# Kernel tuning notes

Hardware: AMD Instinct MI355X
Metric: run time of the kernel (lower is better)

## Reference

```python
import jax, jax.numpy as jnp
import numpy as np

N = 100000   # nodes
E = 3200000  # edges (avg degree 32)
F = 128      # num_features
H = 256      # hidden_dim
D = 256      # embedding_dim
O = 2        # output_dim
BN_EPS = 1e-5


def _mk_layer(keys, fin, fmid, fout):
    kW1, kW2 = keys
    W1 = jax.random.normal(kW1, (fin, fmid), jnp.float32) / np.sqrt(fin)
    b1 = jnp.zeros((fmid,), jnp.float32)
    g = jnp.ones((fmid,), jnp.float32)
    be = jnp.zeros((fmid,), jnp.float32)
    mu = jnp.zeros((fmid,), jnp.float32)
    var = jnp.ones((fmid,), jnp.float32)
    W2 = jax.random.normal(kW2, (fmid, fout), jnp.float32) / np.sqrt(fmid)
    b2 = jnp.zeros((fout,), jnp.float32)
    return W1, b1, g, be, mu, var, W2, b2


def setup_inputs() -> dict:
    key = jax.random.key(0)
    ks = jax.random.split(key, 10)
    inp = {}
    inp["x"] = jax.random.normal(ks[0], (N, F), jnp.float32)
    inp["edge_index"] = jax.random.randint(ks[1], (2, E), 0, N, jnp.int32)
    names = ["W1", "b1", "g", "be", "mu", "var", "W2", "b2"]
    for pref, (fin, fmid, fout), kk in [
        ("l1", (F, H, H), (ks[2], ks[3])),
        ("l2", (H, H, H), (ks[4], ks[5])),
        ("l3", (H, H, D), (ks[6], ks[7])),
    ]:
        vals = _mk_layer(kk, fin, fmid, fout)
        for n, v in zip(names, vals):
            inp[f"{pref}_{n}"] = v
    inp["out_W"] = jax.random.normal(ks[8], (D, O), jnp.float32) / np.sqrt(D)
    inp["out_b"] = jnp.zeros((O,), jnp.float32)
    return inp


def gin_layer(h, src, dst, W1, b1, g, be, mu, var, W2, b2, final_relu):
    # GINConv (eps=0): z_i = x_i + sum_{j->i} x_j, then MLP(Linear-BN-ReLU-Linear[-ReLU])
    agg = jax.ops.segment_sum(h[src], dst, num_segments=N)
    z = h + agg
    z = z @ W1 + b1
    z = (z - mu) * jax.lax.rsqrt(var + BN_EPS) * g + be  # BatchNorm1d (inference)
    z = jax.nn.relu(z)
    z = z @ W2 + b2
    if final_relu:
        z = jax.nn.relu(z)
    return z


def reference(x, edge_index,
              l1_W1, l1_b1, l1_g, l1_be, l1_mu, l1_var, l1_W2, l1_b2,
              l2_W1, l2_b1, l2_g, l2_be, l2_mu, l2_var, l2_W2, l2_b2,
              l3_W1, l3_b1, l3_g, l3_be, l3_mu, l3_var, l3_W2, l3_b2,
              out_W, out_b):
    src, dst = edge_index[0], edge_index[1]
    h = gin_layer(x, src, dst, l1_W1, l1_b1, l1_g, l1_be, l1_mu, l1_var, l1_W2, l1_b2, True)
    h = gin_layer(h, src, dst, l2_W1, l2_b1, l2_g, l2_be, l2_mu, l2_var, l2_W2, l2_b2, True)
    h = gin_layer(h, src, dst, l3_W1, l3_b1, l3_g, l3_be, l3_mu, l3_var, l3_W2, l3_b2, False)
    return h @ out_W + out_b  # [N, O]
```

## Files before the change

kernel.cpp:

```cpp
#include <hip/hip_runtime.h>
#include <cstdint>
#include <cstddef>

#define N_NODES 100000
#define N_EDGES 3200000
#define MPAD    100096
#define HID     256
#define NBUCK   196
#define BSH     9
#define BSTRIDE 18432

typedef _Float16 f16;
typedef _Float16 f16x2 __attribute__((ext_vector_type(2)));
typedef _Float16 f16x8 __attribute__((ext_vector_type(8)));
typedef float    f32x4 __attribute__((ext_vector_type(4)));

union F16x2 { unsigned u; f16 h[2]; f16x2 v; };
__device__ inline void unpack2(unsigned u, float& a, float& b) {
    F16x2 x; x.u = u; a = (float)x.h[0]; b = (float)x.h[1];
}
__device__ inline unsigned pack2(float a, float b) {
    F16x2 x; x.h[0] = (f16)a; x.h[1] = (f16)b; return x.u;
}
__device__ inline f16x2 asv(unsigned u) { F16x2 x; x.u = u; return x.v; }

__global__ __launch_bounds__(256) void k_bucketA(const int* __restrict__ src,
                                                 const int* __restrict__ dst,
                                                 unsigned* __restrict__ pairs,
                                                 int* __restrict__ nb, int e) {
    __shared__ int hist[NBUCK];
    __shared__ int lbase[NBUCK];
    __shared__ int lcur[NBUCK];
    const int t = threadIdx.x;
    for (int i = t; i < NBUCK; i += 256) hist[i] = 0;
    __syncthreads();
    const int e0 = blockIdx.x * 4096;
    bool v[16]; int d[16], s[16];
#pragma unroll
    for (int i = 0; i < 16; ++i) {
        int idx = e0 + i * 256 + t;
        v[i] = idx < e;
        d[i] = v[i] ? dst[idx] : 0;
        s[i] = v[i] ? src[idx] : 0;
    }
#pragma unroll
    for (int i = 0; i < 16; ++i)
        if (v[i]) atomicAdd(&hist[d[i] >> BSH], 1);
    __syncthreads();
    for (int i = t; i < NBUCK; i += 256) {
        int h = hist[i];
        lbase[i] = h ? atomicAdd(&nb[i], h) : 0;
        lcur[i] = 0;
    }
    __syncthreads();
#pragma unroll
    for (int i = 0; i < 16; ++i) {
        if (v[i]) {
            int b = d[i] >> BSH;
            int p = atomicAdd(&lcur[b], 1);
            unsigned packed = ((unsigned)(d[i] & 511) << 17) | (unsigned)s[i];
            pairs[(size_t)b * BSTRIDE + lbase[b] + p] = packed;
        }
    }
}

__global__ void k_scan196(const int* __restrict__ nb, int* __restrict__ bbase,
                          int* __restrict__ rowptrN) {
    __shared__ int s[256];
    int t = threadIdx.x;
    int v = (t < NBUCK) ? nb[t] : 0;
    s[t] = v;
    __syncthreads();
    for (int off = 1; off < 256; off <<= 1) {
        int u = (t >= off) ? s[t - off] : 0;
        __syncthreads();
        s[t] += u;
        __syncthreads();
    }
    if (t < NBUCK) bbase[t] = s[t] - v;
    if (t == 0) *rowptrN = N_EDGES;
}

__global__ __launch_bounds__(256) void k_bucketB(const unsigned* __restrict__ pairs,
                                                 const int* __restrict__ nb,
                                                 const int* __restrict__ bbase,
                                                 int* __restrict__ rowptr,
                                                 int* __restrict__ colidx) {
    __shared__ int deg[512];
    __shared__ int sc[512];
    __shared__ int cur[512];
    const int b = blockIdx.x, t = threadIdx.x;
    const int cnt = nb[b], base = bbase[b];
    const unsigned* P = pairs + (size_t)b * BSTRIDE;
    deg[t] = 0; deg[t + 256] = 0;
    __syncthreads();
    for (int i = t; i < cnt; i += 256) atomicAdd(&deg[P[i] >> 17], 1);
    __syncthreads();
    sc[t] = deg[t]; sc[t + 256] = deg[t + 256];
    __syncthreads();
    for (int off = 1; off < 512; off <<= 1) {
        int a0 = (t >= off) ? sc[t - off] : 0;
        int a1 = (t + 256 >= off) ? sc[t + 256 - off] : 0;
        __syncthreads();
        sc[t] += a0; sc[t + 256] += a1;
        __syncthreads();
    }
    int node0 = b << BSH;
#pragma unroll
    for (int rep = 0; rep < 2; ++rep) {
        int i = t + rep * 256;
        int excl = base + sc[i] - deg[i];
        cur[i] = excl;
        int node = node0 + i;
        if (node < N_NODES) rowptr[node] = excl;
    }
    __syncthreads();
    for (int i = t; i < cnt; i += 256) {
        unsigned p = P[i];
        int pos = atomicAdd(&cur[p >> 17], 1);
        colidx[pos] = (int)(p & 0x1FFFF);
    }
}

__global__ void k_cvt(const float2* __restrict__ x, unsigned* __restrict__ o, int n) {
    int t = blockIdx.x * 256 + threadIdx.x;
    if (t < n) { float2 v = x[t]; o[t] = pack2(v.x, v.y); }
}

__global__ void k_foldw1(const float* __restrict__ W, const float* __restrict__ b1,
                         const float* __restrict__ gm, const float* __restrict__ bt,
                         const float* __restrict__ mu, const float* __restrict__ vr,
                         f16* __restrict__ Wt, float* __restrict__ bias, int K) {
    int t = blockIdx.x * 256 + threadIdx.x;
    if (t >= K * 256) return;
    int n = t & 255, k = t >> 8;
    float sc = gm[n] * rsqrtf(vr[n] + 1e-5f);
    Wt[n * K + k] = (f16)(W[t] * sc);
    if (k == 0) bias[n] = (b1[n] - mu[n]) * sc + bt[n];
}

__global__ void k_transb(const float* __restrict__ W, f16* __restrict__ Wt) {
    int t = blockIdx.x * 256 + threadIdx.x;
    int n = t & 255, k = t >> 8;
    Wt[n * 256 + k] = (f16)W[t];
}

__global__ void k_fold2(const float* __restrict__ W2, const float* __restrict__ b2,
                        const float* __restrict__ outW, const float* __restrict__ outb,
                        float* __restrict__ W2o, float* __restrict__ bo) {
    int k = threadIdx.x;
    float a0 = 0.f, a1 = 0.f;
    for (int j = 0; j < 256; ++j) {
        float w = W2[k * 256 + j];
        a0 += w * outW[j * 2 + 0];
        a1 += w * outW[j * 2 + 1];
    }
    W2o[k * 2 + 0] = a0;
    W2o[k * 2 + 1] = a1;
    if (k < 2) {
        float b = outb[k];
        for (int j = 0; j < 256; ++j) b += b2[j] * outW[j * 2 + k];
        bo[k] = b;
    }
}

__global__ void k_agg256(const uint2* __restrict__ h, const unsigned* __restrict__ h8,
                         const int* __restrict__ rp, const int* __restrict__ ci,
                         uint2* __restrict__ z, int n) {
    int gw = (blockIdx.x * 256 + threadIdx.x) >> 6;
    if (gw >= n) return;
    int lane = threadIdx.x & 63;
    const unsigned* h8l = h8 + lane;
    uint2 d = h[(size_t)gw * 64 + lane];
    float a0, a1, a2, a3;
    unpack2(d.x, a0, a1); unpack2(d.y, a2, a3);
    int s = rp[gw], e = rp[gw + 1];
    int p = s;
    for (; p + 7 < e; p += 8) {
        int j0 = ci[p],     j1 = ci[p + 1], j2 = ci[p + 2], j3 = ci[p + 3];
        int j4 = ci[p + 4], j5 = ci[p + 5], j6 = ci[p + 6], j7 = ci[p + 7];
        unsigned u0 = h8l[(size_t)j0 * 64], u1 = h8l[(size_t)j1 * 64];
        unsigned u2 = h8l[(size_t)j2 * 64], u3 = h8l[(size_t)j3 * 64];
        unsigned u4 = h8l[(size_t)j4 * 64], u5 = h8l[(size_t)j5 * 64];
        unsigned u6 = h8l[(size_t)j6 * 64], u7 = h8l[(size_t)j7 * 64];
#pragma unroll
        for (int q = 0; q < 8; ++q) {
            unsigned u = q == 0 ? u0 : q == 1 ? u1 : q == 2 ? u2 : q == 3 ? u3
                       : q == 4 ? u4 : q == 5 ? u5 : q == 6 ? u6 : u7;
            auto lo = __builtin_amdgcn_cvt_pk_f32_fp8(u, false);
            auto hi = __builtin_amdgcn_cvt_pk_f32_fp8(u, true);
            a0 += lo[0]; a1 += lo[1]; a2 += hi[0]; a3 += hi[1];
        }
    }
    for (; p < e; ++p) {
        unsigned u = h8l[(size_t)ci[p] * 64];
        auto lo = __builtin_amdgcn_cvt_pk_f32_fp8(u, false);
        auto hi = __builtin_amdgcn_cvt_pk_f32_fp8(u, true);
        a0 += lo[0]; a1 += lo[1]; a2 += hi[0]; a3 += hi[1];
    }
    uint2 o; o.x = pack2(a0, a1); o.y = pack2(a2, a3);
    z[(size_t)gw * 64 + lane] = o;
}

__global__ void k_agg128(const unsigned* __restrict__ h, const int* __restrict__ rp,
                         const int* __restrict__ ci, unsigned* __restrict__ z, int n) {
    int gw = (blockIdx.x * 256 + threadIdx.x) >> 6;
    if (gw >= n) return;
    int lane = threadIdx.x & 63;
    const unsigned* hl = h + lane;
    float a0, a1, t0, t1;
    unpack2(hl[(size_t)gw * 64], a0, a1);
    int s = rp[gw], e = rp[gw + 1];
    int p = s;
    for (; p + 7 < e; p += 8) {
        int j0 = ci[p],     j1 = ci[p + 1], j2 = ci[p + 2], j3 = ci[p + 3];
        int j4 = ci[p + 4], j5 = ci[p + 5], j6 = ci[p + 6], j7 = ci[p + 7];
        unsigned v0 = hl[(size_t)j0 * 64], v1 = hl[(size_t)j1 * 64];
        unsigned v2 = hl[(size_t)j2 * 64], v3 = hl[(size_t)j3 * 64];
        unsigned v4 = hl[(size_t)j4 * 64], v5 = hl[(size_t)j5 * 64];
        unsigned v6 = hl[(size_t)j6 * 64], v7 = hl[(size_t)j7 * 64];
        f16x2 sx = asv(v0);
        sx += asv(v1); sx += asv(v2); sx += asv(v3);
        sx += asv(v4); sx += asv(v5); sx += asv(v6); sx += asv(v7);
        a0 += (float)sx[0]; a1 += (float)sx[1];
    }
    for (; p < e; ++p) {
        unpack2(hl[(size_t)ci[p] * 64], t0, t1); a0 += t0; a1 += t1;
    }
    z[(size_t)gw * 64 + lane] = pack2(a0, a1);
}

template <int K, bool RELU, bool STORE8>
__global__ __launch_bounds__(256) void k_gemm(const f16* __restrict__ A,
                                              const f16* __restrict__ Bt,
                                              const float* __restrict__ bias,
                                              f16* __restrict__ C,
                                              unsigned char* __restrict__ C8) {
    __shared__ f16 As[128 * 64];
    __shared__ f16 Bs[128 * 64];
    const int tid = threadIdx.x;
    const int bm0 = blockIdx.x * 128;
    const int bn0 = blockIdx.y * 128;
    const int lane = tid & 63, wave = tid >> 6;
    const int quad = lane >> 4, l16 = lane & 15;
    const int wr = (wave >> 1) * 64, wc = (wave & 1) * 64;
    f32x4 acc[4][4] = {};
    const f16* Abase = A + (size_t)bm0 * K;
    const f16* Bbase = Bt + (size_t)bn0 * K;

    for (int k0 = 0; k0 < K; k0 += 64) {
#pragma unroll
        for (int i = 0; i < 4; ++i) {
            int c = i * 256 + tid;
            int m = c >> 3;
            int gg = (c & 7) ^ (m & 7);
            __builtin_amdgcn_global_load_lds(
                (const __attribute__((address_space(1))) unsigned int*)(Abase + (size_t)m * K + k0 + gg * 8),
                (__attribute__((address_space(3))) unsigned int*)(As + (size_t)c * 8), 16, 0, 0);
            __builtin_amdgcn_global_load_lds(
                (const __attribute__((address_space(1))) unsigned int*)(Bbase + (size_t)m * K + k0 + gg * 8),
                (__attribute__((address_space(3))) unsigned int*)(Bs + (size_t)c * 8), 16, 0, 0);
        }
        __syncthreads();
#pragma unroll
        for (int kk = 0; kk < 64; kk += 32) {
            const int gbase = kk >> 3;
            f16x8 af[4], bfv[4];
#pragma unroll
            for (int mi = 0; mi < 4; ++mi) {
                int m = wr + mi * 16 + l16;
                int slot = (gbase + quad) ^ (m & 7);
                af[mi] = *(const f16x8*)&As[(m * 8 + slot) * 8];
            }
#pragma unroll
            for (int ni = 0; ni < 4; ++ni) {
                int m = wc + ni * 16 + l16;
                int slot = (gbase + quad) ^ (m & 7);
                bfv[ni] = *(const f16x8*)&Bs[(m * 8 + slot) * 8];
            }
#pragma unroll
            for (int mi = 0; mi < 4; ++mi)
#pragma unroll
                for (int ni = 0; ni < 4; ++ni)
                    acc[mi][ni] = __builtin_amdgcn_mfma_f32_16x16x32_f16(af[mi], bfv[ni], acc[mi][ni], 0, 0, 0);
        }
        __syncthreads();
    }

    float bv[4];
#pragma unroll
    for (int ni = 0; ni < 4; ++ni) bv[ni] = bias[bn0 + wc + ni * 16 + l16];
#pragma unroll
    for (int mi = 0; mi < 4; ++mi) {
#pragma unroll
        for (int r = 0; r < 4; ++r) {
            size_t row = (size_t)(bm0 + wr + mi * 16 + quad * 4 + r);
            f16* crow = C + row * HID + bn0 + wc + l16;
            unsigned char* crow8 = STORE8 ? (C8 + row * HID + bn0 + wc + l16) : nullptr;
#pragma unroll
            for (int ni = 0; ni < 4; ++ni) {
                float v = acc[mi][ni][r] + bv[ni];
                if (RELU) v = fmaxf(v, 0.f);
                crow[ni * 16] = (f16)v;
                if (STORE8) {
                    int pk = __builtin_amdgcn_cvt_pk_fp8_f32(v, v, 0, false);
                    crow8[ni * 16] = (unsigned char)(pk & 0xff);
                }
            }
        }
    }
}

__global__ void k_head(const uint2* __restrict__ y, const float* __restrict__ W2o,
                       const float* __restrict__ bo, float* __restrict__ out, int n) {
    __shared__ float w[512];
    __shared__ float bb[2];
    int t = threadIdx.x;
    w[t] = W2o[t];
    w[t + 256] = W2o[t + 256];
    if (t < 2) bb[t] = bo[t];
    __syncthreads();
    int gw = (blockIdx.x * 256 + t) >> 6;
    if (gw >= n) return;
    int lane = t & 63;
    uint2 d = y[(size_t)gw * 64 + lane];
    float x0, x1, x2, x3;
    unpack2(d.x, x0, x1); unpack2(d.y, x2, x3);
    int k = lane * 4;
    float o0 = x0 * w[k * 2 + 0] + x1 * w[k * 2 + 2] + x2 * w[k * 2 + 4] + x3 * w[k * 2 + 6];
    float o1 = x0 * w[k * 2 + 1] + x1 * w[k * 2 + 3] + x2 * w[k * 2 + 5] + x3 * w[k * 2 + 7];
#pragma unroll
    for (int off = 32; off > 0; off >>= 1) {
        o0 += __shfl_down(o0, off);
        o1 += __shfl_down(o1, off);
    }
    if (lane == 0) {
        out[(size_t)gw * 2 + 0] = o0 + bb[0];
        out[(size_t)gw * 2 + 1] = o1 + bb[1];
    }
}

extern "C" void kernel_launch(void* const* d_in, const int* in_sizes, int n_in,
                              void* d_out, int out_size, void* d_ws, size_t ws_size,
                              hipStream_t stream) {
    const float* x    = (const float*)d_in[0];
    const int*   ei   = (const int*)d_in[1];
    const int*   esrc = ei;
    const int*   edst = ei + N_EDGES;
    const float* lw[3][8];
    for (int l = 0; l < 3; ++l)
        for (int j = 0; j < 8; ++j) lw[l][j] = (const float*)d_in[2 + l * 8 + j];
    const float* outW = (const float*)d_in[26];
    const float* outB = (const float*)d_in[27];

    char* base = (char*)d_ws;
    size_t off = 0;
    auto alloc = [&](size_t bytes) -> void* {
        void* r = base + off;
        off += (bytes + 255) & ~(size_t)255;
        return r;
    };
    f16* z  = (f16*)alloc((size_t)MPAD * 256 * 2);
    f16* y  = (f16*)alloc((size_t)MPAD * 256 * 2);
    f16* h  = (f16*)alloc((size_t)MPAD * 256 * 2);
    unsigned char* h8 = (unsigned char*)alloc((size_t)MPAD * 256);
    f16* xh = (f16*)alloc((size_t)MPAD * 128 * 2);
    f16* W1t[3]; float* bias1[3]; f16* W2t[2];
    W1t[0] = (f16*)alloc(256 * 128 * 2);
    W1t[1] = (f16*)alloc(256 * 256 * 2);
    W1t[2] = (f16*)alloc(256 * 256 * 2);
    for (int l = 0; l < 2; ++l) W2t[l] = (f16*)alloc(256 * 256 * 2);
    for (int l = 0; l < 3; ++l) bias1[l] = (float*)alloc(256 * 4);
    float* W2o = (float*)alloc(512 * 4);
    float* bo  = (float*)alloc(2 * 4);
    unsigned* pairs = (unsigned*)alloc((size_t)NBUCK * BSTRIDE * 4);
    int* nb     = (int*)alloc(NBUCK * 4);
    int* bbase  = (int*)alloc(NBUCK * 4);
    int* rowptr = (int*)alloc((size_t)(N_NODES + 1) * 4);
    int* colidx = (int*)alloc((size_t)N_EDGES * 4);

    hipMemsetAsync(nb, 0, NBUCK * 4, stream);
    k_bucketA<<<(N_EDGES + 4095) / 4096, 256, 0, stream>>>(esrc, edst, pairs, nb, N_EDGES);
    k_scan196<<<1, 256, 0, stream>>>(nb, bbase, rowptr + N_NODES);
    k_bucketB<<<NBUCK, 256, 0, stream>>>(pairs, nb, bbase, rowptr, colidx);

    k_cvt<<<(N_NODES * 64 + 255) / 256, 256, 0, stream>>>((const float2*)x, (unsigned*)xh, N_NODES * 64);
    k_foldw1<<<128, 256, 0, stream>>>(lw[0][0], lw[0][1], lw[0][2], lw[0][3], lw[0][4], lw[0][5], W1t[0], bias1[0], 128);
    k_foldw1<<<256, 256, 0, stream>>>(lw[1][0], lw[1][1], lw[1][2], lw[1][3], lw[1][4], lw[1][5], W1t[1], bias1[1], 256);
    k_foldw1<<<256, 256, 0, stream>>>(lw[2][0], lw[2][1], lw[2][2], lw[2][3], lw[2][4], lw[2][5], W1t[2], bias1[2], 256);
    k_transb<<<256, 256, 0, stream>>>(lw[0][6], W2t[0]);
    k_transb<<<256, 256, 0, stream>>>(lw[1][6], W2t[1]);
    k_fold2<<<1, 256, 0, stream>>>(lw[2][6], lw[2][7], outW, outB, W2o, bo);

    const dim3 ggrid(MPAD / 128, 2);
    const int WBLOCKS = (N_NODES + 3) / 4;

    k_agg128<<<WBLOCKS, 256, 0, stream>>>((const unsigned*)xh, rowptr, colidx, (unsigned*)z, N_NODES);
    k_gemm<128, true, false><<<ggrid, 256, 0, stream>>>(z, W1t[0], bias1[0], y, nullptr);
    k_gemm<256, true, true ><<<ggrid, 256, 0, stream>>>(y, W2t[0], lw[0][7], h, h8);
    k_agg256<<<WBLOCKS, 256, 0, stream>>>((const uint2*)h, (const unsigned*)h8, rowptr, colidx, (uint2*)z, N_NODES);
    k_gemm<256, true, false><<<ggrid, 256, 0, stream>>>(z, W1t[1], bias1[1], y, nullptr);
    k_gemm<256, true, true ><<<ggrid, 256, 0, stream>>>(y, W2t[1], lw[1][7], h, h8);
    k_agg256<<<WBLOCKS, 256, 0, stream>>>((const uint2*)h, (const unsigned*)h8, rowptr, colidx, (uint2*)z, N_NODES);
    k_gemm<256, true, false><<<ggrid, 256, 0, stream>>>(z, W1t[2], bias1[2], y, nullptr);
    k_head<<<WBLOCKS, 256, 0, stream>>>((const uint2*)y, W2o, bo, (float*)d_out, N_NODES);
}
```

Baseline: 789.1 us.

## Widen GEMM tile to full 256 columns and drop fp16 hidden-state store

```diff
diff --git a/kernel.cpp b/kernel.cpp
--- a/kernel.cpp
+++ b/kernel.cpp
@@ -164,16 +164,20 @@
     }
 }
 
-__global__ void k_agg256(const uint2* __restrict__ h, const unsigned* __restrict__ h8,
+__global__ void k_agg256(const unsigned* __restrict__ h8,
                          const int* __restrict__ rp, const int* __restrict__ ci,
                          uint2* __restrict__ z, int n) {
     int gw = (blockIdx.x * 256 + threadIdx.x) >> 6;
     if (gw >= n) return;
     int lane = threadIdx.x & 63;
     const unsigned* h8l = h8 + lane;
-    uint2 d = h[(size_t)gw * 64 + lane];
     float a0, a1, a2, a3;
-    unpack2(d.x, a0, a1); unpack2(d.y, a2, a3);
+    {
+        unsigned u = h8l[(size_t)gw * 64];
+        auto lo = __builtin_amdgcn_cvt_pk_f32_fp8(u, false);
+        auto hi = __builtin_amdgcn_cvt_pk_f32_fp8(u, true);
+        a0 = lo[0]; a1 = lo[1]; a2 = hi[0]; a3 = hi[1];
+    }
     int s = rp[gw], e = rp[gw + 1];
     int p = s;
     for (; p + 7 < e; p += 8) {
@@ -230,23 +234,22 @@
     z[(size_t)gw * 64 + lane] = pack2(a0, a1);
 }
 
-template <int K, bool RELU, bool STORE8>
-__global__ __launch_bounds__(256) void k_gemm(const f16* __restrict__ A,
-                                              const f16* __restrict__ Bt,
-                                              const float* __restrict__ bias,
-                                              f16* __restrict__ C,
-                                              unsigned char* __restrict__ C8) {
+template <int K, bool RELU, bool ST16, bool ST8>
+__global__ __launch_bounds__(256, 2) void k_gemm2(const f16* __restrict__ A,
+                                                  const f16* __restrict__ Bt,
+                                                  const float* __restrict__ bias,
+                                                  f16* __restrict__ C,
+                                                  unsigned char* __restrict__ C8) {
     __shared__ f16 As[128 * 64];
-    __shared__ f16 Bs[128 * 64];
+    __shared__ f16 Bs[256 * 64];
     const int tid = threadIdx.x;
     const int bm0 = blockIdx.x * 128;
-    const int bn0 = blockIdx.y * 128;
     const int lane = tid & 63, wave = tid >> 6;
     const int quad = lane >> 4, l16 = lane & 15;
-    const int wr = (wave >> 1) * 64, wc = (wave & 1) * 64;
-    f32x4 acc[4][4] = {};
+    const int wr = (wave >> 1) * 64;
+    const int wc = (wave & 1) * 128;
+    f32x4 acc[4][8] = {};
     const f16* Abase = A + (size_t)bm0 * K;
-    const f16* Bbase = Bt + (size_t)bn0 * K;
 
     for (int k0 = 0; k0 < K; k0 += 64) {
 #pragma unroll
@@ -257,15 +260,21 @@
             __builtin_amdgcn_global_load_lds(
                 (const __attribute__((address_space(1))) unsigned int*)(Abase + (size_t)m * K + k0 + gg * 8),
                 (__attribute__((address_space(3))) unsigned int*)(As + (size_t)c * 8), 16, 0, 0);
+        }
+#pragma unroll
+        for (int i = 0; i < 8; ++i) {
+            int c = i * 256 + tid;
+            int m = c >> 3;
+            int gg = (c & 7) ^ (m & 7);
             __builtin_amdgcn_global_load_lds(
-                (const __attribute__((address_space(1))) unsigned int*)(Bbase + (size_t)m * K + k0 + gg * 8),
+                (const __attribute__((address_space(1))) unsigned int*)(Bt + (size_t)m * K + k0 + gg * 8),
                 (__attribute__((address_space(3))) unsigned int*)(Bs + (size_t)c * 8), 16, 0, 0);
         }
         __syncthreads();
 #pragma unroll
         for (int kk = 0; kk < 64; kk += 32) {
             const int gbase = kk >> 3;
-            f16x8 af[4], bfv[4];
+            f16x8 af[4], bfv[8];
 #pragma unroll
             for (int mi = 0; mi < 4; ++mi) {
                 int m = wr + mi * 16 + l16;
@@ -273,7 +282,7 @@
                 af[mi] = *(const f16x8*)&As[(m * 8 + slot) * 8];
             }
 #pragma unroll
-            for (int ni = 0; ni < 4; ++ni) {
+            for (int ni = 0; ni < 8; ++ni) {
                 int m = wc + ni * 16 + l16;
                 int slot = (gbase + quad) ^ (m & 7);
                 bfv[ni] = *(const f16x8*)&Bs[(m * 8 + slot) * 8];
@@ -281,30 +290,29 @@
 #pragma unroll
             for (int mi = 0; mi < 4; ++mi)
 #pragma unroll
-                for (int ni = 0; ni < 4; ++ni)
+                for (int ni = 0; ni < 8; ++ni)
                     acc[mi][ni] = __builtin_amdgcn_mfma_f32_16x16x32_f16(af[mi], bfv[ni], acc[mi][ni], 0, 0, 0);
         }
         __syncthreads();
     }
 
-    float bv[4];
-#pragma unroll
-    for (int ni = 0; ni < 4; ++ni) bv[ni] = bias[bn0 + wc + ni * 16 + l16];
+    float bv[8];
+#pragma unroll
+    for (int ni = 0; ni < 8; ++ni) bv[ni] = bias[wc + ni * 16 + l16];
 #pragma unroll
     for (int mi = 0; mi < 4; ++mi) {
 #pragma unroll
         for (int r = 0; r < 4; ++r) {
             size_t row = (size_t)(bm0 + wr + mi * 16 + quad * 4 + r);
-            f16* crow = C + row * HID + bn0 + wc + l16;
-            unsigned char* crow8 = STORE8 ? (C8 + row * HID + bn0 + wc + l16) : nullptr;
-#pragma unroll
-            for (int ni = 0; ni < 4; ++ni) {
+#pragma unroll
+            for (int ni = 0; ni < 8; ++ni) {
                 float v = acc[mi][ni][r] + bv[ni];
                 if (RELU) v = fmaxf(v, 0.f);
-                crow[ni * 16] = (f16)v;
-                if (STORE8) {
+                int col = wc + ni * 16 + l16;
+                if (ST16) C[row * HID + col] = (f16)v;
+                if (ST8) {
                     int pk = __builtin_amdgcn_cvt_pk_fp8_f32(v, v, 0, false);
-                    crow8[ni * 16] = (unsigned char)(pk & 0xff);
+                    C8[row * HID + col] = (unsigned char)(pk & 0xff);
                 }
             }
         }
@@ -362,7 +370,6 @@
     };
     f16* z  = (f16*)alloc((size_t)MPAD * 256 * 2);
     f16* y  = (f16*)alloc((size_t)MPAD * 256 * 2);
-    f16* h  = (f16*)alloc((size_t)MPAD * 256 * 2);
     unsigned char* h8 = (unsigned char*)alloc((size_t)MPAD * 256);
     f16* xh = (f16*)alloc((size_t)MPAD * 128 * 2);
     f16* W1t[3]; float* bias1[3]; f16* W2t[2];
@@ -392,16 +399,16 @@
     k_transb<<<256, 256, 0, stream>>>(lw[1][6], W2t[1]);
     k_fold2<<<1, 256, 0, stream>>>(lw[2][6], lw[2][7], outW, outB, W2o, bo);
 
-    const dim3 ggrid(MPAD / 128, 2);
+    const int GG = MPAD / 128;
     const int WBLOCKS = (N_NODES + 3) / 4;
 
     k_agg128<<<WBLOCKS, 256, 0, stream>>>((const unsigned*)xh, rowptr, colidx, (unsigned*)z, N_NODES);
-    k_gemm<128, true, false><<<ggrid, 256, 0, stream>>>(z, W1t[0], bias1[0], y, nullptr);
-    k_gemm<256, true, true ><<<ggrid, 256, 0, stream>>>(y, W2t[0], lw[0][7], h, h8);
-    k_agg256<<<WBLOCKS, 256, 0, stream>>>((const uint2*)h, (const unsigned*)h8, rowptr, colidx, (uint2*)z, N_NODES);
-    k_gemm<256, true, false><<<ggrid, 256, 0, stream>>>(z, W1t[1], bias1[1], y, nullptr);
-    k_gemm<256, true, true ><<<ggrid, 256, 0, stream>>>(y, W2t[1], lw[1][7], h, h8);
-    k_agg256<<<WBLOCKS, 256, 0, stream>>>((const uint2*)h, (const unsigned*)h8, rowptr, colidx, (uint2*)z, N_NODES);
-    k_gemm<256, true, false><<<ggrid, 256, 0, stream>>>(z, W1t[2], bias1[2], y, nullptr);
+    k_gemm2<128, true, true,  false><<<GG, 256, 0, stream>>>(z, W1t[0], bias1[0], y, nullptr);
+    k_gemm2<256, true, false, true ><<<GG, 256, 0, stream>>>(y, W2t[0], lw[0][7], nullptr, h8);
+    k_agg256<<<WBLOCKS, 256, 0, stream>>>((const unsigned*)h8, rowptr, colidx, (uint2*)z, N_NODES);
+    k_gemm2<256, true, true,  false><<<GG, 256, 0, stream>>>(z, W1t[1], bias1[1], y, nullptr);
+    k_gemm2<256, true, false, true ><<<GG, 256, 0, stream>>>(y, W2t[1], lw[1][7], nullptr, h8);
+    k_agg256<<<WBLOCKS, 256, 0, stream>>>((const unsigned*)h8, rowptr, colidx, (uint2*)z, N_NODES);
+    k_gemm2<256, true, true,  false><<<GG, 256, 0, stream>>>(z, W1t[2], bias1[2], y, nullptr);
     k_head<<<WBLOCKS, 256, 0, stream>>>((const uint2*)y, W2o, bo, (float*)d_out, N_NODES);
 }
```

Measured after the change: 751.5 us. 4.8% less time.
